# Kernel optimization log

Hardware: AMD Instinct MI355X
Metric: run time of the kernel (lower is better)

The kernel has to match this reference:

```python
import jax, jax.numpy as jnp
import numpy as np

N_POINTS = 262144
SP_FEAT = 128
HIDDEN = 64
EMBED = 256
NUM_SP = 4096
NUM_SP2 = 256
PAD_LIMIT = 64
MASK_RATIO = 0.6


def setup_inputs() -> dict:
    key = jax.random.key(0)
    ks = jax.random.split(key, 6)
    x = jax.random.normal(ks[0], (N_POINTS, SP_FEAT), jnp.float32)
    # point -> superpoint ids, sorted; force every superpoint non-empty
    idx10 = jax.random.randint(ks[1], (N_POINTS,), 0, NUM_SP)
    idx10 = jnp.sort(idx10.at[:NUM_SP].set(jnp.arange(NUM_SP))).astype(jnp.int32)
    # superpoint -> higher superpoint, balanced (16 per group, < PAD_LIMIT), sorted
    idx21 = ((jnp.arange(NUM_SP) * NUM_SP2) // NUM_SP).astype(jnp.int32)
    # deterministic mask: exactly int(NUM_SP * MASK_RATIO) superpoints masked
    mask_num = int(NUM_SP * MASK_RATIO)
    perm = jax.random.permutation(ks[2], NUM_SP)
    is_masked = jnp.zeros((NUM_SP,), bool).at[perm[:mask_num]].set(True)
    W1 = jax.random.normal(ks[3], (SP_FEAT, HIDDEN), jnp.float32) / np.sqrt(SP_FEAT).astype(np.float32)
    b1 = jnp.zeros((HIDDEN,), jnp.float32)
    W2 = jax.random.normal(ks[4], (HIDDEN, EMBED), jnp.float32) / np.sqrt(HIDDEN).astype(np.float32)
    b2 = jnp.zeros((EMBED,), jnp.float32)
    return {
        "full_features": x,
        "full_super_indices_10": idx10,
        "full_super_indices_21": idx21,
        "is_masked": is_masked,
        "W1": W1, "b1": b1, "W2": W2, "b2": b2,
    }


def _pad_scatter(tokens, idx21, flag):
    # tokens: [NUM_SP, C]; idx21 sorted sp->sp2 ids; flag: [NUM_SP] bool.
    # rank of each flagged superpoint within its sp2 group (in sp order)
    f = flag.astype(jnp.int32)
    cum = jnp.cumsum(f)                                            # inclusive global cumsum
    per_group = jax.ops.segment_sum(f, idx21, num_segments=NUM_SP2)
    prefix = jnp.concatenate([jnp.zeros((1,), jnp.int32), jnp.cumsum(per_group)[:-1]])
    rank = cum - 1 - prefix[idx21]                                 # 0-based slot within group
    slot = jnp.where(flag, rank, PAD_LIMIT)                        # PAD_LIMIT -> dropped
    out = jnp.zeros((NUM_SP2, PAD_LIMIT, tokens.shape[-1]), tokens.dtype)
    return out.at[idx21, slot].set(tokens, mode="drop")


def reference(full_features, full_super_indices_10, full_super_indices_21,
              is_masked, W1, b1, W2, b2):
    # per-point 2-layer MLP (gather is implicit: MLP is pointwise), then segment max
    h = jax.nn.relu(full_features @ W1 + b1)                       # [N, HIDDEN]
    h = jax.nn.relu(h @ W2 + b2)                                   # [N, EMBED]
    tok = jax.ops.segment_max(h, full_super_indices_10, num_segments=NUM_SP)  # [NUM_SP, EMBED]
    remain_tokens = _pad_scatter(tok, full_super_indices_21, ~is_masked)      # [NUM_SP2, PAD, EMBED]
    mask_tokens = _pad_scatter(tok, full_super_indices_21, is_masked)         # [NUM_SP2, PAD, EMBED]
    return (remain_tokens, mask_tokens)
```

## Files before the change

kernel.cpp:

```cpp
#include <hip/hip_runtime.h>
#include <hip/hip_bf16.h>

#define N_POINTS 262144
#define SP_FEAT 128
#define HIDDEN 64
#define EMBED 256
#define NUM_SP 4096
#define NUM_SP2 256
#define PAD_LIMIT 64

typedef __bf16 bf16x8 __attribute__((ext_vector_type(8)));
typedef float floatx4 __attribute__((ext_vector_type(4)));
using bf16 = __hip_bfloat16;

__global__ void prep_kernel(const float* __restrict__ W1, const float* __restrict__ W2,
                            const int* __restrict__ idx10,
                            bf16* __restrict__ W1t, bf16* __restrict__ W2t,
                            int* __restrict__ start) {
    int i = blockIdx.x * blockDim.x + threadIdx.x;
    if (i < HIDDEN * SP_FEAT) {
        int n = i >> 7, k = i & 127;
        W1t[i] = __float2bfloat16(W1[k * HIDDEN + n]);
    } else if (i < HIDDEN * SP_FEAT + EMBED * HIDDEN) {
        int j = i - HIDDEN * SP_FEAT;
        int n = j >> 6, k = j & 63;
        W2t[j] = __float2bfloat16(W2[k * EMBED + n]);
    } else if (i <= HIDDEN * SP_FEAT + EMBED * HIDDEN + NUM_SP) {
        int s = i - (HIDDEN * SP_FEAT + EMBED * HIDDEN);
        if (s == NUM_SP) { start[s] = N_POINTS; return; }
        int a = 0, b = N_POINTS;
        while (a < b) { int m = (a + b) >> 1; if (idx10[m] < s) a = m + 1; else b = m; }
        start[s] = a;
    }
}

__global__ __launch_bounds__(256) void rank_kernel(
    const int* __restrict__ idx21, const void* __restrict__ is_masked,
    int* __restrict__ invR, int* __restrict__ invM) {
    __shared__ int encS;
    const int tid = threadIdx.x;
    if (tid == 0) encS = 0;
    __syncthreads();
    const unsigned char* mb = (const unsigned char*)is_masked;
    const int* mi = (const int*)is_masked;
    int local = 0;
    for (int p = tid; p < NUM_SP; p += 256)
        if ((p & 3) && mb[p]) local = 1;
    if (local) atomicOr(&encS, 1);
    __syncthreads();
    const int e = encS;

    const int g = tid;
    int a = 0, b = NUM_SP;
    while (a < b) { int m = (a + b) >> 1; if (idx21[m] < g) a = m + 1; else b = m; }
    int lo = a;
    b = NUM_SP;
    while (a < b) { int m = (a + b) >> 1; if (idx21[m] < g + 1) a = m + 1; else b = m; }
    int hi = a;
    int nR = 0, nM = 0;
    for (int s = lo; s < hi; ++s) {
        int msk = e ? (int)mb[s] : mi[s];
        if (msk) { if (nM < PAD_LIMIT) invM[g * PAD_LIMIT + nM] = s; nM++; }
        else     { if (nR < PAD_LIMIT) invR[g * PAD_LIMIT + nR] = s; nR++; }
    }
    for (int r = nR; r < PAD_LIMIT; ++r) invR[g * PAD_LIMIT + r] = -1;
    for (int r = nM; r < PAD_LIMIT; ++r) invM[g * PAD_LIMIT + r] = -1;
}

__global__ __launch_bounds__(256) void mlp_segmax_kernel(
    const float* __restrict__ X, const int* __restrict__ start,
    const bf16* __restrict__ W1t, const float* __restrict__ b1,
    const bf16* __restrict__ W2t, const float* __restrict__ b2,
    float* __restrict__ tok)
{
    __shared__ __align__(16) bf16 Xs[64][136];
    __shared__ __align__(16) bf16 H1s[64][72];
    __shared__ float tokS[EMBED];

    const int tid  = threadIdx.x;
    const int lane = tid & 63;
    const int w    = tid >> 6;
    const int l15  = lane & 15;
    const int quad = lane >> 4;
    const int s    = blockIdx.x;

    const int s0 = start[s];
    int cnt = start[s + 1] - s0;
    if (cnt < 1) cnt = 1;
    const int ntiles = (cnt + 63) >> 6;

    bf16x8 bw1[4];
    {
        const bf16* p = W1t + (16 * w + l15) * SP_FEAT + quad * 8;
#pragma unroll
        for (int ks = 0; ks < 4; ++ks) bw1[ks] = *(const bf16x8*)(p + 32 * ks);
    }
    bf16x8 bf2[4][2];
#pragma unroll
    for (int tn = 0; tn < 4; ++tn) {
        const bf16* p = W2t + (64 * w + 16 * tn + l15) * HIDDEN + quad * 8;
#pragma unroll
        for (int ks = 0; ks < 2; ++ks) bf2[tn][ks] = *(const bf16x8*)(p + 32 * ks);
    }
    float b2f[4];
#pragma unroll
    for (int tn = 0; tn < 4; ++tn) b2f[tn] = b2[64 * w + 16 * tn + l15];
    const float b1v = b1[16 * w + l15];

    floatx4 zero4 = {0.f, 0.f, 0.f, 0.f};
    floatx4 macc[4][4];
#pragma unroll
    for (int tm = 0; tm < 4; ++tm)
#pragma unroll
        for (int tn = 0; tn < 4; ++tn)
#pragma unroll
            for (int r = 0; r < 4; ++r) macc[tm][tn][r] = -3e38f;

    for (int t = 0; t < ntiles; ++t) {
        __syncthreads();
#pragma unroll
        for (int i = 0; i < 4; ++i) {
            int c   = tid + 256 * i;
            int row = c >> 4;
            int cc  = (c & 15) * 8;
            int pr  = t * 64 + row;
            if (pr >= cnt) pr = cnt - 1;
            const float* src = X + (size_t)(s0 + pr) * SP_FEAT + cc;
            float4 u0 = *(const float4*)src;
            float4 u1 = *(const float4*)(src + 4);
            union { bf16x8 v; bf16 h[8]; } u;
            u.h[0] = __float2bfloat16(u0.x); u.h[1] = __float2bfloat16(u0.y);
            u.h[2] = __float2bfloat16(u0.z); u.h[3] = __float2bfloat16(u0.w);
            u.h[4] = __float2bfloat16(u1.x); u.h[5] = __float2bfloat16(u1.y);
            u.h[6] = __float2bfloat16(u1.z); u.h[7] = __float2bfloat16(u1.w);
            *(bf16x8*)(&Xs[row][cc]) = u.v;
        }
        __syncthreads();

        floatx4 acc1[4] = {zero4, zero4, zero4, zero4};
#pragma unroll
        for (int ks = 0; ks < 4; ++ks) {
            int k = ks * 32 + quad * 8;
#pragma unroll
            for (int tm = 0; tm < 4; ++tm) {
                bf16x8 a = *(bf16x8*)(&Xs[16 * tm + l15][k]);
                acc1[tm] = __builtin_amdgcn_mfma_f32_16x16x32_bf16(a, bw1[ks], acc1[tm], 0, 0, 0);
            }
        }
#pragma unroll
        for (int tm = 0; tm < 4; ++tm) {
#pragma unroll
            for (int r = 0; r < 4; ++r) {
                float v = acc1[tm][r] + b1v;
                v = v > 0.f ? v : 0.f;
                H1s[16 * tm + quad * 4 + r][16 * w + l15] = __float2bfloat16(v);
            }
        }
        __syncthreads();

#pragma unroll
        for (int tm = 0; tm < 4; ++tm) {
            bf16x8 a0 = *(bf16x8*)(&H1s[16 * tm + l15][quad * 8]);
            bf16x8 a1 = *(bf16x8*)(&H1s[16 * tm + l15][32 + quad * 8]);
#pragma unroll
            for (int tn = 0; tn < 4; ++tn) {
                floatx4 acc = zero4;
                acc = __builtin_amdgcn_mfma_f32_16x16x32_bf16(a0, bf2[tn][0], acc, 0, 0, 0);
                acc = __builtin_amdgcn_mfma_f32_16x16x32_bf16(a1, bf2[tn][1], acc, 0, 0, 0);
#pragma unroll
                for (int r = 0; r < 4; ++r)
                    macc[tm][tn][r] = fmaxf(macc[tm][tn][r], acc[r]);
            }
        }
    }

#pragma unroll
    for (int tn = 0; tn < 4; ++tn) {
        float bst = -3e38f;
#pragma unroll
        for (int tm = 0; tm < 4; ++tm)
#pragma unroll
            for (int r = 0; r < 4; ++r) bst = fmaxf(bst, macc[tm][tn][r]);
        bst = fmaxf(bst, __shfl_xor(bst, 16, 64));
        bst = fmaxf(bst, __shfl_xor(bst, 32, 64));
        float v = bst + b2f[tn];
        v = v > 0.f ? v : 0.f;
        if (quad == 0) tokS[64 * w + 16 * tn + l15] = v;
    }
    __syncthreads();
    tok[(size_t)s * EMBED + tid] = tokS[tid];
}

__global__ __launch_bounds__(256) void scatter_kernel(
    const float* __restrict__ tok, const int* __restrict__ invR,
    const int* __restrict__ invM, float* __restrict__ out)
{
    const int g    = blockIdx.x >> 3;
    const int part = blockIdx.x & 7;
    const int tid  = threadIdx.x;
    float* outR = out + (size_t)g * PAD_LIMIT * EMBED;
    float* outM = out + (size_t)NUM_SP2 * PAD_LIMIT * EMBED + (size_t)g * PAD_LIMIT * EMBED;
#pragma unroll
    for (int rr = 0; rr < 16; ++rr) {
        int row = part * 16 + rr;
        if (row < PAD_LIMIT) {
            int sp = invR[g * PAD_LIMIT + row];
            float v = (sp >= 0) ? tok[(size_t)sp * EMBED + tid] : 0.f;
            outR[row * EMBED + tid] = v;
        } else {
            int r = row - PAD_LIMIT;
            int sp = invM[g * PAD_LIMIT + r];
            float v = (sp >= 0) ? tok[(size_t)sp * EMBED + tid] : 0.f;
            outM[r * EMBED + tid] = v;
        }
    }
}

extern "C" void kernel_launch(void* const* d_in, const int* in_sizes, int n_in,
                              void* d_out, int out_size, void* d_ws, size_t ws_size,
                              hipStream_t stream) {
    (void)in_sizes; (void)n_in; (void)ws_size; (void)out_size;
    const float* X        = (const float*)d_in[0];
    const int* idx10      = (const int*)d_in[1];
    const int* idx21      = (const int*)d_in[2];
    const void* is_masked = (const void*)d_in[3];
    const float* W1       = (const float*)d_in[4];
    const float* b1       = (const float*)d_in[5];
    const float* W2       = (const float*)d_in[6];
    const float* b2       = (const float*)d_in[7];
    float* out            = (float*)d_out;

    char* ws    = (char*)d_ws;
    float* tok  = (float*)ws;
    bf16* W1t   = (bf16*)(ws + (size_t)NUM_SP * EMBED * 4);
    bf16* W2t   = W1t + HIDDEN * SP_FEAT;
    int*  start = (int*)((char*)(W2t + EMBED * HIDDEN));
    int*  invR  = start + (NUM_SP + 2);
    int*  invM  = invR + NUM_SP2 * PAD_LIMIT;

    const int prep_n = HIDDEN * SP_FEAT + EMBED * HIDDEN + NUM_SP + 1;
    prep_kernel<<<(prep_n + 255) / 256, 256, 0, stream>>>(W1, W2, idx10, W1t, W2t, start);
    rank_kernel<<<1, 256, 0, stream>>>(idx21, is_masked, invR, invM);
    mlp_segmax_kernel<<<NUM_SP, 256, 0, stream>>>(X, start, W1t, b1, W2t, b2, tok);
    scatter_kernel<<<NUM_SP2 * 8, 256, 0, stream>>>(tok, invR, invM, out);
}
```

Measured before the change: 265.4 us.

## Tile MLP by fixed 64-point chunks with per-superpoint partial max slots

Switches the MLP+segment-max kernel from one block per superpoint (ragged, with padded tiles) to one block per fixed 64-point chunk. Each block runs the two-layer MLP once, stages outputs in shared memory, and does a run-length max over the sorted superpoint ids. Results go to per-superpoint partial slots, with plain stores for the first three chunks a superpoint spans and atomicMax for any later ones. The scatter kernel then folds the four slots into the final token. This removes the padding waste and load imbalance of ragged segments. The cost is a memset of the partial buffer, a larger workspace, bf16 rounding of outputs before the max, and a serial 64-row scan per thread. The atomicMax on integer bit patterns and the zero-initialised slots rely on the ReLU outputs being non-negative.

```diff
diff --git a/kernel.cpp b/kernel.cpp
--- a/kernel.cpp
+++ b/kernel.cpp
@@ -8,6 +8,8 @@
 #define NUM_SP 4096
 #define NUM_SP2 256
 #define PAD_LIMIT 64
+#define SLOTS 4
+#define OS_STRIDE 268
 
 typedef __bf16 bf16x8 __attribute__((ext_vector_type(8)));
 typedef float floatx4 __attribute__((ext_vector_type(4)));
@@ -68,26 +70,25 @@
 }
 
 __global__ __launch_bounds__(256) void mlp_segmax_kernel(
-    const float* __restrict__ X, const int* __restrict__ start,
+    const float* __restrict__ X, const int* __restrict__ idx10,
+    const int* __restrict__ start,
     const bf16* __restrict__ W1t, const float* __restrict__ b1,
     const bf16* __restrict__ W2t, const float* __restrict__ b2,
-    float* __restrict__ tok)
+    float* __restrict__ partial)
 {
-    __shared__ __align__(16) bf16 Xs[64][136];
+    __shared__ __align__(16) char smemU[64 * OS_STRIDE * 2];
     __shared__ __align__(16) bf16 H1s[64][72];
-    __shared__ float tokS[EMBED];
+    __shared__ int sIdx[64];
+    bf16 (*Xs)[136]      = (bf16(*)[136])smemU;
+    bf16 (*Os)[OS_STRIDE] = (bf16(*)[OS_STRIDE])smemU;
 
     const int tid  = threadIdx.x;
     const int lane = tid & 63;
     const int w    = tid >> 6;
     const int l15  = lane & 15;
     const int quad = lane >> 4;
-    const int s    = blockIdx.x;
-
-    const int s0 = start[s];
-    int cnt = start[s + 1] - s0;
-    if (cnt < 1) cnt = 1;
-    const int ntiles = (cnt + 63) >> 6;
+    const int b    = blockIdx.x;
+    const int m0   = b * 64;
 
     bf16x8 bw1[4];
     {
@@ -107,112 +108,108 @@
     for (int tn = 0; tn < 4; ++tn) b2f[tn] = b2[64 * w + 16 * tn + l15];
     const float b1v = b1[16 * w + l15];
 
+#pragma unroll
+    for (int i = 0; i < 4; ++i) {
+        int c   = tid + 256 * i;
+        int row = c >> 4;
+        int cc  = (c & 15) * 8;
+        const float* src = X + (size_t)(m0 + row) * SP_FEAT + cc;
+        float4 u0 = *(const float4*)src;
+        float4 u1 = *(const float4*)(src + 4);
+        union { bf16x8 v; bf16 h[8]; } u;
+        u.h[0] = __float2bfloat16(u0.x); u.h[1] = __float2bfloat16(u0.y);
+        u.h[2] = __float2bfloat16(u0.z); u.h[3] = __float2bfloat16(u0.w);
+        u.h[4] = __float2bfloat16(u1.x); u.h[5] = __float2bfloat16(u1.y);
+        u.h[6] = __float2bfloat16(u1.z); u.h[7] = __float2bfloat16(u1.w);
+        *(bf16x8*)(&Xs[row][cc]) = u.v;
+    }
+    if (tid < 64) sIdx[tid] = idx10[m0 + tid];
+    __syncthreads();
+
     floatx4 zero4 = {0.f, 0.f, 0.f, 0.f};
-    floatx4 macc[4][4];
-#pragma unroll
-    for (int tm = 0; tm < 4; ++tm)
-#pragma unroll
-        for (int tn = 0; tn < 4; ++tn)
-#pragma unroll
-            for (int r = 0; r < 4; ++r) macc[tm][tn][r] = -3e38f;
-
-    for (int t = 0; t < ntiles; ++t) {
-        __syncthreads();
-#pragma unroll
-        for (int i = 0; i < 4; ++i) {
-            int c   = tid + 256 * i;
-            int row = c >> 4;
-            int cc  = (c & 15) * 8;
-            int pr  = t * 64 + row;
-            if (pr >= cnt) pr = cnt - 1;
-            const float* src = X + (size_t)(s0 + pr) * SP_FEAT + cc;
-            float4 u0 = *(const float4*)src;
-            float4 u1 = *(const float4*)(src + 4);
-            union { bf16x8 v; bf16 h[8]; } u;
-            u.h[0] = __float2bfloat16(u0.x); u.h[1] = __float2bfloat16(u0.y);
-            u.h[2] = __float2bfloat16(u0.z); u.h[3] = __float2bfloat16(u0.w);
-            u.h[4] = __float2bfloat16(u1.x); u.h[5] = __float2bfloat16(u1.y);
-            u.h[6] = __float2bfloat16(u1.z); u.h[7] = __float2bfloat16(u1.w);
-            *(bf16x8*)(&Xs[row][cc]) = u.v;
-        }
-        __syncthreads();
-
-        floatx4 acc1[4] = {zero4, zero4, zero4, zero4};
-#pragma unroll
-        for (int ks = 0; ks < 4; ++ks) {
-            int k = ks * 32 + quad * 8;
-#pragma unroll
-            for (int tm = 0; tm < 4; ++tm) {
-                bf16x8 a = *(bf16x8*)(&Xs[16 * tm + l15][k]);
-                acc1[tm] = __builtin_amdgcn_mfma_f32_16x16x32_bf16(a, bw1[ks], acc1[tm], 0, 0, 0);
+    floatx4 acc1[4] = {zero4, zero4, zero4, zero4};
+#pragma unroll
+    for (int ks = 0; ks < 4; ++ks) {
+        int k = ks * 32 + quad * 8;
+#pragma unroll
+        for (int tm = 0; tm < 4; ++tm) {
+            bf16x8 a = *(bf16x8*)(&Xs[16 * tm + l15][k]);
+            acc1[tm] = __builtin_amdgcn_mfma_f32_16x16x32_bf16(a, bw1[ks], acc1[tm], 0, 0, 0);
+        }
+    }
+#pragma unroll
+    for (int tm = 0; tm < 4; ++tm) {
+#pragma unroll
+        for (int r = 0; r < 4; ++r) {
+            float v = acc1[tm][r] + b1v;
+            v = v > 0.f ? v : 0.f;
+            H1s[16 * tm + quad * 4 + r][16 * w + l15] = __float2bfloat16(v);
+        }
+    }
+    __syncthreads();
+
+#pragma unroll
+    for (int tm = 0; tm < 4; ++tm) {
+        bf16x8 a0 = *(bf16x8*)(&H1s[16 * tm + l15][quad * 8]);
+        bf16x8 a1 = *(bf16x8*)(&H1s[16 * tm + l15][32 + quad * 8]);
+#pragma unroll
+        for (int tn = 0; tn < 4; ++tn) {
+            floatx4 acc = zero4;
+            acc = __builtin_amdgcn_mfma_f32_16x16x32_bf16(a0, bf2[tn][0], acc, 0, 0, 0);
+            acc = __builtin_amdgcn_mfma_f32_16x16x32_bf16(a1, bf2[tn][1], acc, 0, 0, 0);
+#pragma unroll
+            for (int r = 0; r < 4; ++r) {
+                float v = acc[r] + b2f[tn];
+                v = v > 0.f ? v : 0.f;
+                Os[16 * tm + quad * 4 + r][64 * w + 16 * tn + l15] = __float2bfloat16(v);
             }
         }
-#pragma unroll
-        for (int tm = 0; tm < 4; ++tm) {
-#pragma unroll
-            for (int r = 0; r < 4; ++r) {
-                float v = acc1[tm][r] + b1v;
-                v = v > 0.f ? v : 0.f;
-                H1s[16 * tm + quad * 4 + r][16 * w + l15] = __float2bfloat16(v);
+    }
+    __syncthreads();
+
+    {
+        int cur_sp = sIdx[0];
+        float cur  = __bfloat162float(Os[0][tid]);
+        for (int r = 1; r < 64; ++r) {
+            int sp = sIdx[r];
+            float v = __bfloat162float(Os[r][tid]);
+            if (sp != cur_sp) {
+                int slot = b - (start[cur_sp] >> 6);
+                int* dst = (int*)(partial + ((size_t)cur_sp * SLOTS + (slot < 3 ? slot : 3)) * EMBED + tid);
+                if (slot < 3) *(float*)dst = cur;
+                else atomicMax(dst, __float_as_int(cur));
+                cur_sp = sp;
+                cur = v;
+            } else {
+                cur = fmaxf(cur, v);
             }
         }
-        __syncthreads();
-
-#pragma unroll
-        for (int tm = 0; tm < 4; ++tm) {
-            bf16x8 a0 = *(bf16x8*)(&H1s[16 * tm + l15][quad * 8]);
-            bf16x8 a1 = *(bf16x8*)(&H1s[16 * tm + l15][32 + quad * 8]);
-#pragma unroll
-            for (int tn = 0; tn < 4; ++tn) {
-                floatx4 acc = zero4;
-                acc = __builtin_amdgcn_mfma_f32_16x16x32_bf16(a0, bf2[tn][0], acc, 0, 0, 0);
-                acc = __builtin_amdgcn_mfma_f32_16x16x32_bf16(a1, bf2[tn][1], acc, 0, 0, 0);
-#pragma unroll
-                for (int r = 0; r < 4; ++r)
-                    macc[tm][tn][r] = fmaxf(macc[tm][tn][r], acc[r]);
-            }
-        }
-    }
-
-#pragma unroll
-    for (int tn = 0; tn < 4; ++tn) {
-        float bst = -3e38f;
-#pragma unroll
-        for (int tm = 0; tm < 4; ++tm)
-#pragma unroll
-            for (int r = 0; r < 4; ++r) bst = fmaxf(bst, macc[tm][tn][r]);
-        bst = fmaxf(bst, __shfl_xor(bst, 16, 64));
-        bst = fmaxf(bst, __shfl_xor(bst, 32, 64));
-        float v = bst + b2f[tn];
-        v = v > 0.f ? v : 0.f;
-        if (quad == 0) tokS[64 * w + 16 * tn + l15] = v;
-    }
-    __syncthreads();
-    tok[(size_t)s * EMBED + tid] = tokS[tid];
+        int slot = b - (start[cur_sp] >> 6);
+        int* dst = (int*)(partial + ((size_t)cur_sp * SLOTS + (slot < 3 ? slot : 3)) * EMBED + tid);
+        if (slot < 3) *(float*)dst = cur;
+        else atomicMax(dst, __float_as_int(cur));
+    }
 }
 
 __global__ __launch_bounds__(256) void scatter_kernel(
-    const float* __restrict__ tok, const int* __restrict__ invR,
+    const float* __restrict__ partial, const int* __restrict__ invR,
     const int* __restrict__ invM, float* __restrict__ out)
 {
-    const int g    = blockIdx.x >> 3;
-    const int part = blockIdx.x & 7;
+    const int bb   = blockIdx.x;
+    const int g    = bb & (NUM_SP2 - 1);
+    const int slab = bb >> 8;
     const int tid  = threadIdx.x;
-    float* outR = out + (size_t)g * PAD_LIMIT * EMBED;
-    float* outM = out + (size_t)NUM_SP2 * PAD_LIMIT * EMBED + (size_t)g * PAD_LIMIT * EMBED;
-#pragma unroll
-    for (int rr = 0; rr < 16; ++rr) {
-        int row = part * 16 + rr;
-        if (row < PAD_LIMIT) {
-            int sp = invR[g * PAD_LIMIT + row];
-            float v = (sp >= 0) ? tok[(size_t)sp * EMBED + tid] : 0.f;
-            outR[row * EMBED + tid] = v;
-        } else {
-            int r = row - PAD_LIMIT;
-            int sp = invM[g * PAD_LIMIT + r];
-            float v = (sp >= 0) ? tok[(size_t)sp * EMBED + tid] : 0.f;
-            outM[r * EMBED + tid] = v;
-        }
+    const int* tab = slab ? invM : invR;
+    float* o = out + ((size_t)slab * NUM_SP2 + g) * PAD_LIMIT * EMBED;
+#pragma unroll 4
+    for (int row = 0; row < PAD_LIMIT; ++row) {
+        int sp = tab[g * PAD_LIMIT + row];
+        float v = 0.f;
+        if (sp >= 0) {
+            const float* p = partial + (size_t)sp * SLOTS * EMBED + tid;
+            v = fmaxf(fmaxf(p[0], p[EMBED]), fmaxf(p[2 * EMBED], p[3 * EMBED]));
+        }
+        o[row * EMBED + tid] = v;
     }
 }
 
@@ -230,17 +227,20 @@
     const float* b2       = (const float*)d_in[7];
     float* out            = (float*)d_out;
 
-    char* ws    = (char*)d_ws;
-    float* tok  = (float*)ws;
-    bf16* W1t   = (bf16*)(ws + (size_t)NUM_SP * EMBED * 4);
-    bf16* W2t   = W1t + HIDDEN * SP_FEAT;
-    int*  start = (int*)((char*)(W2t + EMBED * HIDDEN));
-    int*  invR  = start + (NUM_SP + 2);
-    int*  invM  = invR + NUM_SP2 * PAD_LIMIT;
+    char* ws      = (char*)d_ws;
+    float* partial = (float*)ws;
+    bf16* W1t     = (bf16*)(ws + (size_t)NUM_SP * SLOTS * EMBED * 4);
+    bf16* W2t     = W1t + HIDDEN * SP_FEAT;
+    int*  start   = (int*)((char*)(W2t + EMBED * HIDDEN));
+    int*  invR    = start + (NUM_SP + 2);
+    int*  invM    = invR + NUM_SP2 * PAD_LIMIT;
+
+    hipMemsetAsync(partial, 0, (size_t)NUM_SP * SLOTS * EMBED * sizeof(float), stream);
 
     const int prep_n = HIDDEN * SP_FEAT + EMBED * HIDDEN + NUM_SP + 1;
     prep_kernel<<<(prep_n + 255) / 256, 256, 0, stream>>>(W1, W2, idx10, W1t, W2t, start);
     rank_kernel<<<1, 256, 0, stream>>>(idx21, is_masked, invR, invM);
-    mlp_segmax_kernel<<<NUM_SP, 256, 0, stream>>>(X, start, W1t, b1, W2t, b2, tok);
-    scatter_kernel<<<NUM_SP2 * 8, 256, 0, stream>>>(tok, invR, invM, out);
-}
+    mlp_segmax_kernel<<<N_POINTS / 64, 256, 0, stream>>>(
+        X, idx10, start, W1t, b1, W2t, b2, partial);
+    scatter_kernel<<<NUM_SP2 * 2, 256, 0, stream>>>(partial, invR, invM, out);
+}
```

Result: slower. 272.5 us (+2.7%).
